# Kernel optimization log

Hardware: AMD Instinct MI355X
Metric: run time of the kernel (lower is better)

Reference implementation:

```python
import jax, jax.numpy as jnp
import numpy as np

B, N, H, W = 8, 16384, 64, 64
CTX, OUT, ST = 32, 2, 1
HID = [516, 256, 128, 64, 32, 16]
IN_SIZE = CTX + 2 + ST + OUT  # 37


def _bilinear_sample(img, coord):
    """torch F.grid_sample, mode=bilinear, padding=zeros, align_corners=False.
    img: [B,C,H,W]; coord: [B,N,2] (x,y in [-1,1]). Returns [B,C,N]."""
    _, _, Hh, Ww = img.shape
    gx = (coord[..., 0] + 1.0) * (Ww * 0.5) - 0.5
    gy = (coord[..., 1] + 1.0) * (Hh * 0.5) - 0.5
    x0 = jnp.floor(gx)
    y0 = jnp.floor(gy)
    wx1 = gx - x0
    wy1 = gy - y0

    def tap(xi, yi, w):
        valid = (xi >= 0) & (xi < Ww) & (yi >= 0) & (yi < Hh)
        xc = jnp.clip(xi, 0, Ww - 1).astype(jnp.int32)
        yc = jnp.clip(yi, 0, Hh - 1).astype(jnp.int32)
        vals = jax.vmap(lambda im, y, x: im[:, y, x])(img, yc, xc)  # [B,C,N]
        return vals * (w * valid)[:, None, :]

    return (tap(x0, y0, (1 - wx1) * (1 - wy1))
            + tap(x0 + 1, y0, wx1 * (1 - wy1))
            + tap(x0, y0 + 1, (1 - wx1) * wy1)
            + tap(x0 + 1, y0 + 1, wx1 * wy1))


def _layer_shapes():
    shapes = [(IN_SIZE, HID[0])]
    for i in range(len(HID) - 1):
        shapes.append((HID[i] + IN_SIZE, HID[i + 1]))
    shapes.append((HID[-1], OUT))
    return shapes


def setup_inputs():
    key = jax.random.key(0)
    ks = jax.random.split(key, 4 + 7)
    inp = {
        "lr_fields": jax.random.normal(ks[0], (B, OUT, H, W), jnp.float32),
        "context_grid": jax.random.normal(ks[1], (B, CTX, H, W), jnp.float32),
        "hr_eps": jax.random.normal(ks[2], (B, H, W), jnp.float32),
        "coord": jax.random.uniform(ks[3], (B, N, 2), jnp.float32, -1.0, 1.0),
    }
    for j, (fi, fo) in enumerate(_layer_shapes()):
        inp[f"W{j}"] = jax.random.normal(ks[4 + j], (fi, fo), jnp.float32) / np.sqrt(fi)
        inp[f"b{j}"] = jnp.zeros((fo,), jnp.float32)
    return inp


def reference(lr_fields, context_grid, hr_eps, coord,
              W0, b0, W1, b1, W2, b2, W3, b3, W4, b4, W5, b5, W6, b6):
    # original permutes (0,1,3,2) before grid_sample -> swap spatial axes
    ctx_pts = _bilinear_sample(jnp.swapaxes(context_grid, 2, 3), coord)  # [B,CTX,N]
    lr_pts = _bilinear_sample(jnp.swapaxes(lr_fields, 2, 3), coord)      # [B,OUT,N]
    eps_pts = _bilinear_sample(jnp.swapaxes(hr_eps[:, None], 2, 3), coord)  # [B,1,N]
    x_in = jnp.concatenate([
        jnp.transpose(ctx_pts, (0, 2, 1)),
        coord,
        jnp.transpose(lr_pts, (0, 2, 1)),
        jnp.transpose(eps_pts, (0, 2, 1)),
    ], axis=2)  # [B,N,37]
    x = jax.nn.relu(x_in @ W0 + b0)
    for Wl, bl in ((W1, b1), (W2, b2), (W3, b3), (W4, b4), (W5, b5)):
        x = jax.nn.relu(jnp.concatenate([x, x_in], axis=2) @ Wl + bl)
    return x @ W6 + b6  # [B,N,2]
```

## Files before the change

kernel.cpp:

```cpp
#include <hip/hip_runtime.h>


#define NTH     1024
#define NWAVES  16
#define MPTS    64
#define MTILES  (MPTS / 16)
#define SROW    616
#define XIN_OFF 0
#define HSEG    64
#define NPOINTS (8 * 16384)
#define GRIDX   (NPOINTS / MPTS)
#define LDSBYTES (MPTS * SROW * 2)

typedef short          short8  __attribute__((ext_vector_type(8)));
typedef short          short4v __attribute__((ext_vector_type(4)));
typedef float          f32x4   __attribute__((ext_vector_type(4)));
typedef unsigned short u16;

__device__ __forceinline__ u16 f2bf(float f) {
    unsigned int u = __builtin_bit_cast(unsigned int, f);
    u += 0x7fffu + ((u >> 16) & 1u);
    return (u16)(u >> 16);
}

__constant__ int pk_base8[8] = {0, 4224, 23680, 28800, 30336, 30848, 31040, 31104};
__constant__ int pk_ks[7]    = {2, 19, 10, 6, 4, 3, 1};
__constant__ int pk_khp[7]   = {0, 544, 256, 128, 64, 32, 32};
__constant__ int pk_kact[7]  = {0, 516, 256, 128, 64, 32, 16};
__constant__ int pk_nact[7]  = {516, 256, 128, 64, 32, 16, 2};

struct WPtrs { const float* W[7]; };

__global__ void pack_weights(WPtrs wp, u16* __restrict__ out)
{
    const int f = blockIdx.x * blockDim.x + threadIdx.x;
    if (f >= 31104) return;
    int l = 0;
    while (l < 6 && f >= pk_base8[l + 1]) ++l;
    const int r    = f - pk_base8[l];
    const int lane = r & 63;
    const int t    = r >> 6;
    const int ks   = pk_ks[l];
    const int s    = t % ks;
    const int nt   = t / ks;
    const int n    = nt * 16 + (lane & 15);
    const int k0   = s * 32 + (lane >> 4) * 8;
    const int nact = pk_nact[l];
    const int khp  = pk_khp[l];
    const int kact = pk_kact[l];
    const float* W = wp.W[l];

    union { short8 v; u16 e[8]; } frag;
#pragma unroll
    for (int j = 0; j < 8; ++j) {
        const int k = k0 + j;
        float v = 0.0f;
        if (n < nact) {
            if (k < khp) {
                if (k < kact) v = W[k * nact + n];
            } else {
                const int xr = k - khp;
                if (xr < 37) v = W[(kact + xr) * nact + n];
            }
        }
        frag.e[j] = f2bf(v);
    }
    *(short8*)(out + (size_t)f * 8) = frag.v;
}

struct MainParams {
    const float* lr;
    const float* ctx;
    const float* eps;
    const float* coord;
    const float* Bb[7];
    const u16*   wpack;
    float*       out;
};

template<int NACT, bool RELU>
__device__ __forceinline__ void store_nt(const f32x4* accm,
                                         const float* __restrict__ bias,
                                         u16* __restrict__ s_act,
                                         int nt, int mbase, int lm, int lq)
{
    const int bn = nt * 16 + lq * 4;
    float bv[4];
    if (bn + 4 <= NACT) {
        const f32x4 b4 = *(const f32x4*)(bias + bn);
        bv[0] = b4[0]; bv[1] = b4[1]; bv[2] = b4[2]; bv[3] = b4[3];
    } else {
#pragma unroll
        for (int r = 0; r < 4; ++r)
            bv[r] = (bn + r < NACT) ? bias[bn + r] : 0.f;
    }
#pragma unroll
    for (int m = 0; m < 2; ++m) {
        short4v o;
#pragma unroll
        for (int r = 0; r < 4; ++r) {
            float v = accm[m][r] + bv[r];
            if (RELU) v = fmaxf(v, 0.f);
            o[r] = (short)f2bf(v);
        }
        *(short4v*)(s_act + (size_t)((mbase + m) * 16 + lm) * SROW + HSEG + bn) = o;
    }
}

template<int KHP, int NT, int NACT, int LBASE,
         bool XIN, bool RELU, bool GOUT, bool IPBAR>
__device__ __forceinline__ void mlayer(const u16* __restrict__ wpack,
                                       const float* __restrict__ bias,
                                       u16* __restrict__ s_act,
                                       float* __restrict__ gout, int p0,
                                       int wave, int lane)
{
    constexpr int KHS = KHP / 32;
    constexpr int KS  = KHS + (XIN ? 2 : 0);
    const int lm = lane & 15;
    const int lq = lane >> 4;
    const int mg = wave & 1;
    const int ng = wave >> 1;
    const int mbase = mg * 2;

    const u16* arow0 = s_act + (size_t)((mbase * 16) + lm) * SROW + lq * 8;
    const u16* arow1 = arow0 + (size_t)16 * SROW;
    const u16* wl = wpack + LBASE + lane * 8;

#define ABOFF(s_) (((s_) < KHS) ? (HSEG + (s_) * 32) : (XIN_OFF + ((s_) - KHS) * 32))

    if constexpr (IPBAR) {
        const int nt0 = ng, nt1 = ng + 8;
        const bool act0 = nt0 < NT;
        const bool act1 = nt1 < NT;
        f32x4 acc[2][2];
#pragma unroll
        for (int i = 0; i < 2; ++i)
#pragma unroll
            for (int m = 0; m < 2; ++m)
                acc[i][m] = (f32x4){0.f, 0.f, 0.f, 0.f};

        if (act0) {
            const u16* bp0 = wl + (size_t)nt0 * KS * 512;
            const u16* bp1 = wl + (size_t)nt1 * KS * 512;
#pragma unroll
            for (int s = 0; s < KS; ++s) {
                const int ab = ABOFF(s);
                const short8 a0 = *(const short8*)(arow0 + ab);
                const short8 a1 = *(const short8*)(arow1 + ab);
                const short8 w0 = *(const short8*)(bp0 + (size_t)s * 512);
                acc[0][0] = __builtin_amdgcn_mfma_f32_16x16x32_bf16(w0, a0, acc[0][0], 0, 0, 0);
                acc[0][1] = __builtin_amdgcn_mfma_f32_16x16x32_bf16(w0, a1, acc[0][1], 0, 0, 0);
                if (act1) {
                    const short8 w1 = *(const short8*)(bp1 + (size_t)s * 512);
                    acc[1][0] = __builtin_amdgcn_mfma_f32_16x16x32_bf16(w1, a0, acc[1][0], 0, 0, 0);
                    acc[1][1] = __builtin_amdgcn_mfma_f32_16x16x32_bf16(w1, a1, acc[1][1], 0, 0, 0);
                }
            }
        }
        __syncthreads();
        if (act0) store_nt<NACT, RELU>(acc[0], bias, s_act, nt0, mbase, lm, lq);
        if (act1) store_nt<NACT, RELU>(acc[1], bias, s_act, nt1, mbase, lm, lq);
    } else {
        for (int g = 0;; ++g) {
            const int nt0 = ng + 16 * g;
            if (nt0 >= NT) break;
            const int nt1 = nt0 + 8;
            const bool act1 = nt1 < NT;
            f32x4 acc[2][2];
#pragma unroll
            for (int i = 0; i < 2; ++i)
#pragma unroll
                for (int m = 0; m < 2; ++m)
                    acc[i][m] = (f32x4){0.f, 0.f, 0.f, 0.f};

            const u16* bp0 = wl + (size_t)nt0 * KS * 512;
            const u16* bp1 = wl + (size_t)nt1 * KS * 512;
#pragma unroll
            for (int s = 0; s < KS; ++s) {
                const int ab = ABOFF(s);
                const short8 a0 = *(const short8*)(arow0 + ab);
                const short8 a1 = *(const short8*)(arow1 + ab);
                const short8 w0 = *(const short8*)(bp0 + (size_t)s * 512);
                acc[0][0] = __builtin_amdgcn_mfma_f32_16x16x32_bf16(w0, a0, acc[0][0], 0, 0, 0);
                acc[0][1] = __builtin_amdgcn_mfma_f32_16x16x32_bf16(w0, a1, acc[0][1], 0, 0, 0);
                if (act1) {
                    const short8 w1 = *(const short8*)(bp1 + (size_t)s * 512);
                    acc[1][0] = __builtin_amdgcn_mfma_f32_16x16x32_bf16(w1, a0, acc[1][0], 0, 0, 0);
                    acc[1][1] = __builtin_amdgcn_mfma_f32_16x16x32_bf16(w1, a1, acc[1][1], 0, 0, 0);
                }
            }

            if (GOUT) {
                if (lq == 0) {
                    const float b0 = bias[0], b1 = bias[1];
#pragma unroll
                    for (int m = 0; m < 2; ++m) {
                        float2 o;
                        o.x = acc[0][m][0] + b0;
                        o.y = acc[0][m][1] + b1;
                        *(float2*)(gout + (size_t)(p0 + (mbase + m) * 16 + lm) * 2) = o;
                    }
                }
            } else {
                store_nt<NACT, RELU>(acc[0], bias, s_act, nt0, mbase, lm, lq);
                if (act1)
                    store_nt<NACT, RELU>(acc[1], bias, s_act, nt1, mbase, lm, lq);
            }
        }
    }
#undef ABOFF
}

__global__ __launch_bounds__(NTH, 8)
void cont_decoder_mfma(MainParams p)
{
    extern __shared__ u16 s_act[];
    __shared__ int   s_x0[MPTS], s_y0[MPTS];
    __shared__ float s_wx[MPTS], s_wy[MPTS];

    const int tid  = threadIdx.x;
    const int wave = tid >> 6;
    const int lane = tid & 63;
    const int p0   = blockIdx.x * MPTS;
    const int b    = p0 >> 14;

    for (int i = tid; i < MPTS * 43; i += NTH) {
        const int pt = i / 43, c = i % 43;
        const int col = (c < 27) ? (37 + c) : (592 + (c - 27));
        s_act[pt * SROW + col] = 0;
    }

    if (tid < MPTS) {
        const int pt = p0 + tid;
        const float cx = p.coord[2 * pt];
        const float cy = p.coord[2 * pt + 1];
        const float gx = (cx + 1.0f) * 32.0f - 0.5f;
        const float gy = (cy + 1.0f) * 32.0f - 0.5f;
        const float fx0 = floorf(gx), fy0 = floorf(gy);
        s_x0[tid] = (int)fx0;
        s_y0[tid] = (int)fy0;
        s_wx[tid] = gx - fx0;
        s_wy[tid] = gy - fy0;
        s_act[tid * SROW + 32] = f2bf(cx);
        s_act[tid * SROW + 33] = f2bf(cy);
    }
    __syncthreads();

    for (int idx = tid; idx < MPTS * 35; idx += NTH) {
        const int t = idx / 35;
        const int c = idx % 35;
        const float* base;
        int col;
        if (c < 32)      { base = p.ctx + (size_t)(b * 32 + c) * 4096;       col = c; }
        else if (c < 34) { base = p.lr  + (size_t)(b * 2 + (c - 32)) * 4096; col = 34 + (c - 32); }
        else             { base = p.eps + (size_t)b * 4096;                   col = 36; }

        const int   x0 = s_x0[t], y0 = s_y0[t];
        const float wx = s_wx[t], wy = s_wy[t];
        const int x1 = x0 + 1, y1 = y0 + 1;
        const bool xv0 = (x0 >= 0) & (x0 < 64);
        const bool xv1 = (x1 >= 0) & (x1 < 64);
        const bool yv0 = (y0 >= 0) & (y0 < 64);
        const bool yv1 = (y1 >= 0) & (y1 < 64);
        const int xc0 = min(max(x0, 0), 63), xc1 = min(max(x1, 0), 63);
        const int yc0 = min(max(y0, 0), 63), yc1 = min(max(y1, 0), 63);

        const float w00 = (1.0f - wx) * (1.0f - wy) * ((xv0 && yv0) ? 1.0f : 0.0f);
        const float w10 = wx * (1.0f - wy)          * ((xv1 && yv0) ? 1.0f : 0.0f);
        const float w01 = (1.0f - wx) * wy          * ((xv0 && yv1) ? 1.0f : 0.0f);
        const float w11 = wx * wy                   * ((xv1 && yv1) ? 1.0f : 0.0f);

        const float val = w00 * base[xc0 * 64 + yc0]
                        + w10 * base[xc1 * 64 + yc0]
                        + w01 * base[xc0 * 64 + yc1]
                        + w11 * base[xc1 * 64 + yc1];
        s_act[t * SROW + col] = f2bf(val);
    }
    __syncthreads();

    mlayer<  0, 33, 516, 0,      true,  true,  false, false>(p.wpack, p.Bb[0], s_act, nullptr, p0, wave, lane);
    __syncthreads();
    mlayer<544, 16, 256, 33792,  true,  true,  false, true >(p.wpack, p.Bb[1], s_act, nullptr, p0, wave, lane);
    __syncthreads();
    mlayer<256,  8, 128, 189440, true,  true,  false, true >(p.wpack, p.Bb[2], s_act, nullptr, p0, wave, lane);
    __syncthreads();
    mlayer<128,  4,  64, 230400, true,  true,  false, true >(p.wpack, p.Bb[3], s_act, nullptr, p0, wave, lane);
    __syncthreads();
    mlayer< 64,  2,  32, 242688, true,  true,  false, true >(p.wpack, p.Bb[4], s_act, nullptr, p0, wave, lane);
    __syncthreads();
    mlayer< 32,  1,  16, 246784, true,  true,  false, true >(p.wpack, p.Bb[5], s_act, nullptr, p0, wave, lane);
    __syncthreads();
    mlayer< 32,  1,   2, 248320, false, false, true,  false>(p.wpack, p.Bb[6], s_act, p.out,   p0, wave, lane);
}

extern "C" void kernel_launch(void* const* d_in, const int* in_sizes, int n_in,
                              void* d_out, int out_size, void* d_ws, size_t ws_size,
                              hipStream_t stream)
{
    WPtrs wp;
    for (int l = 0; l < 7; ++l) wp.W[l] = (const float*)d_in[4 + 2 * l];

    MainParams p;
    p.lr    = (const float*)d_in[0];
    p.ctx   = (const float*)d_in[1];
    p.eps   = (const float*)d_in[2];
    p.coord = (const float*)d_in[3];
    for (int l = 0; l < 7; ++l) p.Bb[l] = (const float*)d_in[5 + 2 * l];
    p.wpack = (const u16*)d_ws;
    p.out   = (float*)d_out;

    hipFuncSetAttribute((const void*)cont_decoder_mfma,
                        hipFuncAttributeMaxDynamicSharedMemorySize, LDSBYTES);

    hipLaunchKernelGGL(pack_weights, dim3(122), dim3(256), 0, stream, wp, (u16*)d_ws);
    hipLaunchKernelGGL(cont_decoder_mfma, dim3(GRIDX), dim3(NTH), LDSBYTES, stream, p);
}
```

Baseline: 211.2 us.

## Repack feature grids channel-last in workspace before bilinear gathering

Adds a pre-pass kernel that transposes the context, lr and eps grids into a per-pixel channel-last layout with stride 38 in the workspace. The main kernel's bilinear sampling then reads all 35 channels of one tap from adjacent addresses instead of 35 separate planes. This targets scattered gather traffic at the cost of an extra kernel launch and one extra read and write of the grids. It falls back to the old path if the workspace is too small.

```diff
diff --git a/kernel.cpp b/kernel.cpp
--- a/kernel.cpp
+++ b/kernel.cpp
@@ -11,6 +11,8 @@
 #define NPOINTS (8 * 16384)
 #define GRIDX   (NPOINTS / MPTS)
 #define LDSBYTES (MPTS * SROW * 2)
+#define CLSTRIDE 38
+#define CLOFF   524288
 
 typedef short          short8  __attribute__((ext_vector_type(8)));
 typedef short          short4v __attribute__((ext_vector_type(4)));
@@ -68,6 +70,28 @@
     *(short8*)(out + (size_t)f * 8) = frag.v;
 }
 
+struct RPk { const float* ctx; const float* lr; const float* eps; float* cl; };
+
+__global__ void repack_cl(RPk q)
+{
+    __shared__ float ls[64 * CLSTRIDE];
+    const int b = blockIdx.x >> 6;
+    const int x = blockIdx.x & 63;
+    for (int i = threadIdx.x; i < 64 * CLSTRIDE; i += 256) ls[i] = 0.f;
+    __syncthreads();
+    for (int i = threadIdx.x; i < 35 * 64; i += 256) {
+        const int c = i / 64, y = i % 64;
+        float v; int slot;
+        if (c < 32)      { v = q.ctx[(((size_t)b * 32 + c) * 64 + x) * 64 + y]; slot = c; }
+        else if (c < 34) { v = q.lr [(((size_t)b * 2 + (c - 32)) * 64 + x) * 64 + y]; slot = 34 + (c - 32); }
+        else             { v = q.eps[(((size_t)b) * 64 + x) * 64 + y];          slot = 36; }
+        ls[y * CLSTRIDE + slot] = v;
+    }
+    __syncthreads();
+    float* out = q.cl + ((size_t)b * 64 + x) * 64 * CLSTRIDE;
+    for (int i = threadIdx.x; i < 64 * CLSTRIDE; i += 256) out[i] = ls[i];
+}
+
 struct MainParams {
     const float* lr;
     const float* ctx;
@@ -75,6 +99,8 @@
     const float* coord;
     const float* Bb[7];
     const u16*   wpack;
+    const float* cl;
+    int          clok;
     float*       out;
 };
 
@@ -247,35 +273,65 @@
     }
     __syncthreads();
 
-    for (int idx = tid; idx < MPTS * 35; idx += NTH) {
-        const int t = idx / 35;
-        const int c = idx % 35;
-        const float* base;
-        int col;
-        if (c < 32)      { base = p.ctx + (size_t)(b * 32 + c) * 4096;       col = c; }
-        else if (c < 34) { base = p.lr  + (size_t)(b * 2 + (c - 32)) * 4096; col = 34 + (c - 32); }
-        else             { base = p.eps + (size_t)b * 4096;                   col = 36; }
-
-        const int   x0 = s_x0[t], y0 = s_y0[t];
-        const float wx = s_wx[t], wy = s_wy[t];
-        const int x1 = x0 + 1, y1 = y0 + 1;
-        const bool xv0 = (x0 >= 0) & (x0 < 64);
-        const bool xv1 = (x1 >= 0) & (x1 < 64);
-        const bool yv0 = (y0 >= 0) & (y0 < 64);
-        const bool yv1 = (y1 >= 0) & (y1 < 64);
-        const int xc0 = min(max(x0, 0), 63), xc1 = min(max(x1, 0), 63);
-        const int yc0 = min(max(y0, 0), 63), yc1 = min(max(y1, 0), 63);
-
-        const float w00 = (1.0f - wx) * (1.0f - wy) * ((xv0 && yv0) ? 1.0f : 0.0f);
-        const float w10 = wx * (1.0f - wy)          * ((xv1 && yv0) ? 1.0f : 0.0f);
-        const float w01 = (1.0f - wx) * wy          * ((xv0 && yv1) ? 1.0f : 0.0f);
-        const float w11 = wx * wy                   * ((xv1 && yv1) ? 1.0f : 0.0f);
-
-        const float val = w00 * base[xc0 * 64 + yc0]
-                        + w10 * base[xc1 * 64 + yc0]
-                        + w01 * base[xc0 * 64 + yc1]
-                        + w11 * base[xc1 * 64 + yc1];
-        s_act[t * SROW + col] = f2bf(val);
+    if (p.clok) {
+        const float* cl = p.cl + (size_t)b * 64 * 64 * CLSTRIDE;
+        for (int idx = tid; idx < MPTS * 35; idx += NTH) {
+            const int t = idx / 35;
+            const int c = idx % 35;
+            const int col = (c < 32) ? c : 34 + (c - 32);
+
+            const int   x0 = s_x0[t], y0 = s_y0[t];
+            const float wx = s_wx[t], wy = s_wy[t];
+            const int x1 = x0 + 1, y1 = y0 + 1;
+            const bool xv0 = (x0 >= 0) & (x0 < 64);
+            const bool xv1 = (x1 >= 0) & (x1 < 64);
+            const bool yv0 = (y0 >= 0) & (y0 < 64);
+            const bool yv1 = (y1 >= 0) & (y1 < 64);
+            const int xc0 = min(max(x0, 0), 63), xc1 = min(max(x1, 0), 63);
+            const int yc0 = min(max(y0, 0), 63), yc1 = min(max(y1, 0), 63);
+
+            const float w00 = (1.0f - wx) * (1.0f - wy) * ((xv0 && yv0) ? 1.0f : 0.0f);
+            const float w10 = wx * (1.0f - wy)          * ((xv1 && yv0) ? 1.0f : 0.0f);
+            const float w01 = (1.0f - wx) * wy          * ((xv0 && yv1) ? 1.0f : 0.0f);
+            const float w11 = wx * wy                   * ((xv1 && yv1) ? 1.0f : 0.0f);
+
+            const float val = w00 * cl[(size_t)(xc0 * 64 + yc0) * CLSTRIDE + col]
+                            + w10 * cl[(size_t)(xc1 * 64 + yc0) * CLSTRIDE + col]
+                            + w01 * cl[(size_t)(xc0 * 64 + yc1) * CLSTRIDE + col]
+                            + w11 * cl[(size_t)(xc1 * 64 + yc1) * CLSTRIDE + col];
+            s_act[t * SROW + col] = f2bf(val);
+        }
+    } else {
+        for (int idx = tid; idx < MPTS * 35; idx += NTH) {
+            const int t = idx / 35;
+            const int c = idx % 35;
+            const float* base;
+            int col;
+            if (c < 32)      { base = p.ctx + (size_t)(b * 32 + c) * 4096;       col = c; }
+            else if (c < 34) { base = p.lr  + (size_t)(b * 2 + (c - 32)) * 4096; col = 34 + (c - 32); }
+            else             { base = p.eps + (size_t)b * 4096;                   col = 36; }
+
+            const int   x0 = s_x0[t], y0 = s_y0[t];
+            const float wx = s_wx[t], wy = s_wy[t];
+            const int x1 = x0 + 1, y1 = y0 + 1;
+            const bool xv0 = (x0 >= 0) & (x0 < 64);
+            const bool xv1 = (x1 >= 0) & (x1 < 64);
+            const bool yv0 = (y0 >= 0) & (y0 < 64);
+            const bool yv1 = (y1 >= 0) & (y1 < 64);
+            const int xc0 = min(max(x0, 0), 63), xc1 = min(max(x1, 0), 63);
+            const int yc0 = min(max(y0, 0), 63), yc1 = min(max(y1, 0), 63);
+
+            const float w00 = (1.0f - wx) * (1.0f - wy) * ((xv0 && yv0) ? 1.0f : 0.0f);
+            const float w10 = wx * (1.0f - wy)          * ((xv1 && yv0) ? 1.0f : 0.0f);
+            const float w01 = (1.0f - wx) * wy          * ((xv0 && yv1) ? 1.0f : 0.0f);
+            const float w11 = wx * wy                   * ((xv1 && yv1) ? 1.0f : 0.0f);
+
+            const float val = w00 * base[xc0 * 64 + yc0]
+                            + w10 * base[xc1 * 64 + yc0]
+                            + w01 * base[xc0 * 64 + yc1]
+                            + w11 * base[xc1 * 64 + yc1];
+            s_act[t * SROW + col] = f2bf(val);
+        }
     }
     __syncthreads();
 
@@ -300,6 +356,9 @@
 {
     WPtrs wp;
     for (int l = 0; l < 7; ++l) wp.W[l] = (const float*)d_in[4 + 2 * l];
+
+    const size_t cl_bytes = (size_t)8 * 64 * 64 * CLSTRIDE * 4;
+    const bool clok = ws_size >= (size_t)CLOFF + cl_bytes;
 
     MainParams p;
     p.lr    = (const float*)d_in[0];
@@ -308,11 +367,19 @@
     p.coord = (const float*)d_in[3];
     for (int l = 0; l < 7; ++l) p.Bb[l] = (const float*)d_in[5 + 2 * l];
     p.wpack = (const u16*)d_ws;
+    p.cl    = (const float*)((const char*)d_ws + CLOFF);
+    p.clok  = clok ? 1 : 0;
     p.out   = (float*)d_out;
 
     hipFuncSetAttribute((const void*)cont_decoder_mfma,
                         hipFuncAttributeMaxDynamicSharedMemorySize, LDSBYTES);
 
     hipLaunchKernelGGL(pack_weights, dim3(122), dim3(256), 0, stream, wp, (u16*)d_ws);
+    if (clok) {
+        RPk q;
+        q.ctx = p.ctx; q.lr = p.lr; q.eps = p.eps;
+        q.cl  = (float*)((char*)d_ws + CLOFF);
+        hipLaunchKernelGGL(repack_cl, dim3(512), dim3(256), 0, stream, q);
+    }
     hipLaunchKernelGGL(cont_decoder_mfma, dim3(GRIDX), dim3(NTH), LDSBYTES, stream, p);
 }
```

Measured after the change: 187.0 us. 1.13x faster.
